# Kernel tuning notes

Measured on AMD Instinct MI355X. Metric: run time of the kernel, lower is better.

Reference implementation:

```python
import jax, jax.numpy as jnp
from jax import lax
import numpy as np

B, N, C_IN = 2, 4096, 64
NPOINT, K1, K2, S, K3 = 1024, 32, 16, 128, 16
C1, CD, CW1, CW2 = 64, 32, 96, 128


def _pw(x, W, b):
    # pointwise (1x1) conv + ReLU; x: (..., Cin), W: (Cout, Cin)
    return jax.nn.relu(jnp.einsum('...c,oc->...o', x, W) + b)


def _gather(x, idx):
    # x: (B, N, ...), idx: (B, ...) int -> fancy-gather along point dim
    return jax.vmap(lambda a, i: a[i])(x, idx)


def _fps(xyz, m):
    # furthest point sampling -> (B, m) int32 indices (non-differentiable)
    xyz = lax.stop_gradient(xyz)
    b, n, _ = xyz.shape
    d0 = jnp.full((b, n), 1e10, xyz.dtype)
    i0 = jnp.zeros((b,), jnp.int32)

    def body(carry, _):
        dists, last = carry
        lp = jnp.take_along_axis(xyz, last[:, None, None], axis=1)  # (B,1,3)
        dists = jnp.minimum(dists, jnp.sum((xyz - lp) ** 2, axis=-1))
        nxt = jnp.argmax(dists, axis=-1).astype(jnp.int32)
        return (dists, nxt), nxt

    (_, _), rest = lax.scan(body, (d0, i0), None, length=m - 1)
    return jnp.concatenate([i0[None, :], rest], axis=0).T  # (B,m)


def _knn(ref, q, k, ref_comp=None, q_comp=None):
    # k nearest ref points for each query point; optional same-component
    # constraint (knnquery with comp) via large distance penalty.
    ref = lax.stop_gradient(ref)
    q = lax.stop_gradient(q)
    d = jnp.sum((q[:, :, None, :] - ref[:, None, :, :]) ** 2, axis=-1)  # (B,M,N)
    if ref_comp is not None:
        d = d + jnp.where(q_comp[:, :, None] != ref_comp[:, None, :], 1e9, 0.0).astype(d.dtype)
    _, idx = lax.top_k(-d, k)
    return idx


def _indices(xyz, comp):
    cidx = _fps(xyz, NPOINT)                 # furthestsampling
    new_xyz = _gather(xyz, cidx)             # gathering
    new_comp = _gather(comp, cidx)
    idx1 = _knn(xyz, new_xyz, K1)            # grouper
    idx2 = _knn(new_xyz, new_xyz, K2, new_comp, new_comp)   # sp_knnquery
    sp_idx = _fps(new_xyz, S)
    sp_xyz = _gather(new_xyz, sp_idx)
    sp_comp = _gather(new_comp, sp_idx)
    idx_sp = _knn(new_xyz, sp_xyz, K3, new_comp, sp_comp)   # sp_knnquery_for_3rd
    idx3 = _knn(new_xyz, new_xyz, K2, new_comp, new_comp)   # sp_knnquery3
    return cidx, new_comp, idx1, idx2, idx_sp, idx3


def _forward(xyz, features, cidx, idx1, idx2, idx_sp, idx3, p):
    new_xyz = _gather(xyz, cidx)                             # (B,M,3)
    feat1 = _pw(features, p['W1d'], p['b1d'])                # mlps_1d -> (B,N,C1)
    center = _gather(feat1, cidx)                            # (B,M,C1)

    # --- stage 1: grouper over raw points ---
    d_xyz1 = _gather(xyz, idx1) - new_xyz[:, :, None, :]     # (B,M,K1,3)
    o_fea1 = _gather(feat1, idx1)                            # (B,M,K1,C1)
    w1 = _pw(jnp.concatenate([d_xyz1, o_fea1 - center[:, :, None, :]], -1), p['Ww1'], p['bw1'])
    c_fea1 = w1.max(axis=2)                                  # maxpool over K1
    w1s = jax.nn.softmax(w1, axis=2)                         # softmax over neighbors
    d1m = _pw(d_xyz1, p['Wdx1'], p['bdx1'])
    g_fea1 = jnp.sum(jnp.concatenate([d1m, o_fea1], -1) * w1s, axis=2)   # (B,M,96)

    # --- stage 2: comp-constrained knn among sampled points ---
    d_xyz2 = _gather(new_xyz, idx2) - new_xyz[:, :, None, :]  # (B,M,K2,3)
    o_fea2 = _gather(g_fea1, idx2)                            # (B,M,K2,96)
    d_fea2 = jnp.concatenate([o_fea2 - g_fea1[:, :, None, :], d_xyz2], -1)  # (B,M,K2,99)
    d2m = _pw(d_xyz2, p['Wdx2'], p['bdx2'])
    w2 = _pw(d_fea2, p['Ww2'], p['bw2'])                      # (B,M,K2,128)
    c_fea2 = w2.max(axis=2)
    w2s = jax.nn.softmax(w2, axis=2)
    g_fea2 = jnp.sum(jnp.concatenate([d2m, o_fea2], -1) * w2s, axis=2)   # (B,M,128)

    # --- stage 3: superpoint pooling, dense point<->superpoint attention ---
    sp_fea = _gather(c_fea2, idx_sp).max(axis=2)              # (B,S,128)
    d_fea3 = sp_fea[:, None, :, :] - c_fea2[:, :, None, :]    # (B,M,S,128)
    w3 = _pw(d_fea3, p['Ww3'], p['bw3'])
    w3s = jax.nn.softmax(w3, axis=2)                          # softmax over S
    g_fea3 = jnp.sum(c_fea2[:, :, None, :] * w3s, axis=2)     # (B,M,128)

    # --- stage 3b: knn group over g_fea2 ---
    d_xyz3 = _gather(new_xyz, idx3) - new_xyz[:, :, None, :]
    o_fea3 = _gather(g_fea2, idx3)
    d_fea3b = jnp.concatenate([o_fea3 - g_fea2[:, :, None, :], d_xyz3], -1)  # (B,M,K2,131)
    local_point_fea = _pw(d_fea3b, p['Wsp3'], p['bsp3']).max(axis=2)         # (B,M,128)

    fea3 = jnp.concatenate([g_fea3, local_point_fea, g_fea2, c_fea2, g_fea1, c_fea1, center], -1)  # (B,M,768)
    new_features = _pw(fea3, p['Wnew'], p['bnew'])            # (B,M,256)
    return new_xyz, jnp.swapaxes(new_features, 1, 2)          # (B,256,M) channel-first like torch


def setup_inputs():
    key = jax.random.key(0)
    ks = jax.random.split(key, 12)
    w = lambda k, s: jax.random.normal(k, s, jnp.float32) * 0.1
    return {
        'xyz': jax.random.normal(ks[0], (B, N, 3), jnp.float32),
        'features': jax.random.normal(ks[1], (B, N, C_IN), jnp.float32),
        'comp': jax.random.randint(ks[2], (B, N), 0, 8, jnp.int32),
        'W1d': w(ks[3], (C1, C_IN)), 'b1d': jnp.zeros((C1,), jnp.float32),
        'Wdx1': w(ks[4], (CD, 3)), 'bdx1': jnp.zeros((CD,), jnp.float32),
        'Ww1': w(ks[5], (CW1, 3 + C1)), 'bw1': jnp.zeros((CW1,), jnp.float32),
        'Wdx2': w(ks[6], (CD, 3)), 'bdx2': jnp.zeros((CD,), jnp.float32),
        'Ww2': w(ks[7], (CW2, CW1 + 3)), 'bw2': jnp.zeros((CW2,), jnp.float32),
        'Ww3': w(ks[8], (CW2, CW2)), 'bw3': jnp.zeros((CW2,), jnp.float32),
        'Wsp3': w(ks[9], (CW2, CW2 + 3)), 'bsp3': jnp.zeros((CW2,), jnp.float32),
        'Wnew': w(ks[10], (256, 4 * CW2 + 2 * CW1 + C1)), 'bnew': jnp.zeros((256,), jnp.float32),
    }


def reference(xyz, features, comp, W1d, b1d, Wdx1, bdx1, Ww1, bw1, Wdx2, bdx2, Ww2, bw2, Ww3, bw3, Wsp3, bsp3, Wnew, bnew):
    p = {'W1d': W1d, 'b1d': b1d, 'Wdx1': Wdx1, 'bdx1': bdx1, 'Ww1': Ww1, 'bw1': bw1,
         'Wdx2': Wdx2, 'bdx2': bdx2, 'Ww2': Ww2, 'bw2': bw2, 'Ww3': Ww3, 'bw3': bw3,
         'Wsp3': Wsp3, 'bsp3': bsp3, 'Wnew': Wnew, 'bnew': bnew}
    cidx, new_comp, idx1, idx2, idx_sp, idx3 = _indices(xyz, comp)
    new_xyz, new_features = _forward(xyz, features, cidx, idx1, idx2, idx_sp, idx3, p)
    return new_xyz, new_features, new_comp
```

## Files before the change

### kernel.cpp

```cpp
#include <hip/hip_runtime.h>
#include <hip/hip_bf16.h>

#define B_   2
#define N_   4096
#define M_   1024
#define K1_  32
#define K2_  16
#define C1_  64
#define CW1_ 96
#define CW2_ 128
#define CO_  256
#define F3_  768


__device__ __forceinline__ float dist3e(float ax, float ay, float az,
                                        float bx, float by, float bz) {
    float dx = __fsub_rn(ax, bx);
    float dy = __fsub_rn(ay, by);
    float dz = __fsub_rn(az, bz);
    return __fadd_rn(__fadd_rn(__fmul_rn(dx, dx), __fmul_rn(dy, dy)), __fmul_rn(dz, dz));
}

#define DPP_F32_MAX(v, ctrl)                                                        \
    (v) = fmaxf((v), __int_as_float(__builtin_amdgcn_update_dpp(                    \
              __float_as_int(v), __float_as_int(v), (ctrl), 0xf, 0xf, false)))
#define DPP_U32_MIN(v, ctrl)                                                        \
    {                                                                               \
        unsigned _t = (unsigned)__builtin_amdgcn_update_dpp(                        \
            (int)(v), (int)(v), (ctrl), 0xf, 0xf, false);                           \
        (v) = (v) < _t ? (v) : _t;                                                  \
    }

__device__ __forceinline__ float wave_max_f32(float v) {
    DPP_F32_MAX(v, 0x111);
    DPP_F32_MAX(v, 0x112);
    DPP_F32_MAX(v, 0x114);
    DPP_F32_MAX(v, 0x118);
    DPP_F32_MAX(v, 0x142);
    DPP_F32_MAX(v, 0x143);
    return __int_as_float(__builtin_amdgcn_readlane(__float_as_int(v), 63));
}

__device__ __forceinline__ unsigned wave_min_u32(unsigned v) {
    DPP_U32_MIN(v, 0x111);
    DPP_U32_MIN(v, 0x112);
    DPP_U32_MIN(v, 0x114);
    DPP_U32_MIN(v, 0x118);
    DPP_U32_MIN(v, 0x142);
    DPP_U32_MIN(v, 0x143);
    return (unsigned)__builtin_amdgcn_readlane((int)v, 63);
}

__global__ __launch_bounds__(512) void k_fps(const float* __restrict__ xyz,
        const int* __restrict__ comp, int* __restrict__ cidx,
        float* __restrict__ newxyz, int* __restrict__ newcomp,
        float* __restrict__ out_xyz, float* __restrict__ out_comp) {
    __shared__ float sx[N_], sy[N_], sz[N_];
    __shared__ unsigned long long spk[2][8];
    __shared__ int scid[M_];
    const int b = blockIdx.x;
    const int t = threadIdx.x;
    const int lane = t & 63, wv = t >> 6;
    const float* xb = xyz + (size_t)b * N_ * 3;
    for (int i = t; i < N_; i += 512) {
        sx[i] = xb[i * 3 + 0];
        sy[i] = xb[i * 3 + 1];
        sz[i] = xb[i * 3 + 2];
    }
    if (t == 0) scid[0] = 0;
    __syncthreads();
    float px[8], py[8], pz[8], pd[8];
    #pragma unroll
    for (int j = 0; j < 8; ++j) {
        const int p = j * 512 + t;
        px[j] = sx[p]; py[j] = sy[p]; pz[j] = sz[p];
        pd[j] = 1e10f;
    }
    int last = 0;
    for (int it = 1; it < M_; ++it) {
        const float lx = sx[last], ly = sy[last], lz = sz[last];
        #pragma unroll
        for (int j = 0; j < 8; ++j)
            pd[j] = fminf(pd[j], dist3e(px[j], py[j], pz[j], lx, ly, lz));
        float bd = pd[0]; int bj = 0;
        #pragma unroll
        for (int j = 1; j < 8; ++j) if (pd[j] > bd) { bd = pd[j]; bj = j; }
        const int bi = bj * 512 + t;
        const float mw = wave_max_f32(bd);
        unsigned cand = (bd == mw) ? (unsigned)bi : 0xffffffffu;
        const unsigned wi = wave_min_u32(cand);
        const int pb = it & 1;
        if (lane == 0)
            spk[pb][wv] = ((unsigned long long)__float_as_uint(mw) << 32) | (unsigned)(~wi);
        __syncthreads();
        unsigned long long g = spk[pb][0];
        #pragma unroll
        for (int w = 1; w < 8; ++w) {
            const unsigned long long x = spk[pb][w];
            g = x > g ? x : g;
        }
        last = (int)(~(unsigned)(g & 0xffffffffULL));
        if (t == 0) scid[it] = last;
    }
    __syncthreads();
    for (int m = t; m < M_; m += 512) {
        const int idx = scid[m];
        cidx[b * M_ + m] = idx;
        const float vx = sx[idx], vy = sy[idx], vz = sz[idx];
        newxyz[(size_t)(b * M_ + m) * 3 + 0] = vx;
        newxyz[(size_t)(b * M_ + m) * 3 + 1] = vy;
        newxyz[(size_t)(b * M_ + m) * 3 + 2] = vz;
        out_xyz[(size_t)(b * M_ + m) * 3 + 0] = vx;
        out_xyz[(size_t)(b * M_ + m) * 3 + 1] = vy;
        out_xyz[(size_t)(b * M_ + m) * 3 + 2] = vz;
        const int c = comp[b * N_ + idx];
        newcomp[b * M_ + m] = c;
        out_comp[b * M_ + m] = (float)c;
    }
}

__global__ __launch_bounds__(256) void k_feat1(const float* __restrict__ feats,
        const float* __restrict__ W1d, const float* __restrict__ b1d,
        float* __restrict__ feat1) {
    __shared__ float swt[C1_][C1_];
    __shared__ float sxr[4][C1_];
    const int t = threadIdx.x;
    const int o = t & 63, r = t >> 6;
    const size_t rb = (size_t)blockIdx.x * 4;
    for (int i = t; i < C1_ * C1_; i += 256) swt[i & 63][i >> 6] = W1d[i];
    for (int i = t; i < 4 * C1_; i += 256)
        sxr[i >> 6][i & 63] = feats[(rb + (i >> 6)) * C1_ + (i & 63)];
    __syncthreads();
    float acc = b1d[o];
    #pragma unroll
    for (int c = 0; c < C1_; ++c) acc += sxr[r][c] * swt[c][o];
    feat1[(rb + r) * C1_ + o] = fmaxf(acc, 0.f);
}

__global__ __launch_bounds__(256) void k_knn1(const float* __restrict__ xyz,
        const float* __restrict__ newxyz, int* __restrict__ idx1) {
    __shared__ float sx[N_], sy[N_], sz[N_];
    const int b = blockIdx.y;
    const int t = threadIdx.x, lane = t & 63, wv = t >> 6;
    const float* xb = xyz + (size_t)b * N_ * 3;
    for (int i = t; i < N_; i += 256) {
        sx[i] = xb[i * 3 + 0]; sy[i] = xb[i * 3 + 1]; sz[i] = xb[i * 3 + 2];
    }
    __syncthreads();
    const int m = blockIdx.x * 4 + wv;
    const float qx = newxyz[(size_t)(b * M_ + m) * 3 + 0];
    const float qy = newxyz[(size_t)(b * M_ + m) * 3 + 1];
    const float qz = newxyz[(size_t)(b * M_ + m) * 3 + 2];
    unsigned long long dp[64];
    #pragma unroll
    for (int j = 0; j < 64; ++j) {
        const int p = j * 64 + lane;
        const float v = dist3e(sx[p], sy[p], sz[p], qx, qy, qz);
        dp[j] = ((unsigned long long)__float_as_uint(v) << 32) | (unsigned)(p + 1);
    }
    unsigned long long lastk = 0ULL;
    int* op = idx1 + (size_t)(b * M_ + m) * K1_;
    for (int pass = 0; pass < K1_; ++pass) {
        unsigned long long best = ~0ULL;
        #pragma unroll
        for (int j = 0; j < 64; ++j) {
            const unsigned long long x = dp[j];
            if (x > lastk && x < best) best = x;
        }
        #pragma unroll
        for (int s = 32; s; s >>= 1) {
            const unsigned long long o2 = __shfl_xor(best, s, 64);
            best = o2 < best ? o2 : best;
        }
        if (lane == 0) op[pass] = (int)((unsigned)(best & 0xffffffffULL)) - 1;
        lastk = best;
    }
}

__global__ __launch_bounds__(256) void k_knn2(const float* __restrict__ newxyz,
        const int* __restrict__ newcomp, int* __restrict__ idx2) {
    __shared__ float sx[M_], sy[M_], sz[M_];
    __shared__ int scp[M_];
    const int b = blockIdx.y;
    const int t = threadIdx.x, lane = t & 63, wv = t >> 6;
    for (int i = t; i < M_; i += 256) {
        sx[i] = newxyz[(size_t)(b * M_ + i) * 3 + 0];
        sy[i] = newxyz[(size_t)(b * M_ + i) * 3 + 1];
        sz[i] = newxyz[(size_t)(b * M_ + i) * 3 + 2];
        scp[i] = newcomp[b * M_ + i];
    }
    __syncthreads();
    const int m = blockIdx.x * 4 + wv;
    const float qx = sx[m], qy = sy[m], qz = sz[m];
    const int qc = scp[m];
    unsigned long long dp[16];
    #pragma unroll
    for (int j = 0; j < 16; ++j) {
        const int p = j * 64 + lane;
        float dd = dist3e(sx[p], sy[p], sz[p], qx, qy, qz);
        if (scp[p] != qc) dd = __fadd_rn(dd, 1e9f);
        dp[j] = ((unsigned long long)__float_as_uint(dd) << 32) | (unsigned)(p + 1);
    }
    unsigned long long lastk = 0ULL;
    int* op = idx2 + (size_t)(b * M_ + m) * K2_;
    for (int pass = 0; pass < K2_; ++pass) {
        unsigned long long best = ~0ULL;
        #pragma unroll
        for (int j = 0; j < 16; ++j) {
            const unsigned long long x = dp[j];
            if (x > lastk && x < best) best = x;
        }
        #pragma unroll
        for (int s = 32; s; s >>= 1) {
            const unsigned long long o2 = __shfl_xor(best, s, 64);
            best = o2 < best ? o2 : best;
        }
        if (lane == 0) op[pass] = (int)((unsigned)(best & 0xffffffffULL)) - 1;
        lastk = best;
    }
}

__global__ __launch_bounds__(128) void k_stage1(const float* __restrict__ xyz,
        const float* __restrict__ feat1, const float* __restrict__ newxyz,
        const int* __restrict__ cidx, const int* __restrict__ idx1,
        const float* __restrict__ Ww1, const float* __restrict__ bw1,
        const float* __restrict__ Wdx1, const float* __restrict__ bdx1,
        float* __restrict__ gfea1, float* __restrict__ cfea1) {
    __shared__ float sdx[K1_][3];
    __shared__ float sof[K1_][C1_];
    __shared__ float sdf[K1_][C1_];
    __shared__ float sct[C1_];
    const int bm = blockIdx.x;
    const int b = bm >> 10;
    const int t = threadIdx.x;
    const int* iq = idx1 + (size_t)bm * K1_;
    const int ci = cidx[bm];
    if (t < C1_) sct[t] = feat1[((size_t)b * N_ + ci) * C1_ + t];
    for (int i = t; i < K1_ * C1_; i += 128) {
        const int k = i >> 6, c = i & 63;
        sof[k][c] = feat1[((size_t)b * N_ + iq[k]) * C1_ + c];
    }
    const float qx = newxyz[(size_t)bm * 3 + 0];
    const float qy = newxyz[(size_t)bm * 3 + 1];
    const float qz = newxyz[(size_t)bm * 3 + 2];
    if (t < K1_ * 3) {
        const int k = t / 3, c = t % 3;
        const float q = (c == 0) ? qx : ((c == 1) ? qy : qz);
        sdx[k][c] = xyz[((size_t)b * N_ + iq[k]) * 3 + c] - q;
    }
    __syncthreads();
    for (int i = t; i < K1_ * C1_; i += 128) {
        const int k = i >> 6, c = i & 63;
        sdf[k][c] = sof[k][c] - sct[c];
    }
    __syncthreads();
    const int o = t;
    if (o < CW1_) {
        float wr[67];
        const float* wp = Ww1 + o * 67;
        #pragma unroll
        for (int j = 0; j < 67; ++j) wr[j] = wp[j];
        const float bias = bw1[o];
        float w1v[K1_];
        #pragma unroll
        for (int k = 0; k < K1_; ++k) {
            float acc = bias + sdx[k][0] * wr[0] + sdx[k][1] * wr[1] + sdx[k][2] * wr[2];
            #pragma unroll
            for (int c = 0; c < C1_; ++c) acc += sdf[k][c] * wr[3 + c];
            w1v[k] = fmaxf(acc, 0.f);
        }
        float mx = w1v[0];
        #pragma unroll
        for (int k = 1; k < K1_; ++k) mx = fmaxf(mx, w1v[k]);
        cfea1[(size_t)bm * CW1_ + o] = mx;
        float dw0 = 0.f, dw1 = 0.f, dw2 = 0.f, db = 0.f;
        if (o < 32) {
            dw0 = Wdx1[o * 3 + 0]; dw1 = Wdx1[o * 3 + 1]; dw2 = Wdx1[o * 3 + 2];
            db = bdx1[o];
        }
        float s = 0.f, acc = 0.f;
        #pragma unroll
        for (int k = 0; k < K1_; ++k) {
            const float e = __expf(w1v[k] - mx);
            s += e;
            float val;
            if (o < 32) val = fmaxf(db + sdx[k][0] * dw0 + sdx[k][1] * dw1 + sdx[k][2] * dw2, 0.f);
            else        val = sof[k][o - 32];
            acc += val * e;
        }
        gfea1[(size_t)bm * CW1_ + o] = acc / s;
    }
}

__global__ __launch_bounds__(128) void k_stage2(const float* __restrict__ newxyz,
        const float* __restrict__ gfea1, const int* __restrict__ idx2,
        const float* __restrict__ Ww2, const float* __restrict__ bw2,
        const float* __restrict__ Wdx2, const float* __restrict__ bdx2,
        float* __restrict__ gfea2, float* __restrict__ cfea2) {
    __shared__ float sdx[K2_][3];
    __shared__ float sof[K2_][CW1_];
    __shared__ float sdf[K2_][CW1_];
    __shared__ float sg1[CW1_];
    const int bm = blockIdx.x;
    const int b = bm >> 10;
    const int t = threadIdx.x;
    const int* iq = idx2 + (size_t)bm * K2_;
    if (t < CW1_) sg1[t] = gfea1[(size_t)bm * CW1_ + t];
    for (int i = t; i < K2_ * CW1_; i += 128) {
        const int k = i / CW1_, c = i % CW1_;
        sof[k][c] = gfea1[((size_t)b * M_ + iq[k]) * CW1_ + c];
    }
    const float qx = newxyz[(size_t)bm * 3 + 0];
    const float qy = newxyz[(size_t)bm * 3 + 1];
    const float qz = newxyz[(size_t)bm * 3 + 2];
    if (t < K2_ * 3) {
        const int k = t / 3, c = t % 3;
        const float q = (c == 0) ? qx : ((c == 1) ? qy : qz);
        sdx[k][c] = newxyz[((size_t)b * M_ + iq[k]) * 3 + c] - q;
    }
    __syncthreads();
    for (int i = t; i < K2_ * CW1_; i += 128) {
        const int k = i / CW1_, c = i % CW1_;
        sdf[k][c] = sof[k][c] - sg1[c];
    }
    __syncthreads();
    const int o = t;
    float wr[99];
    const float* wp = Ww2 + o * 99;
    #pragma unroll
    for (int j = 0; j < 99; ++j) wr[j] = wp[j];
    const float bias = bw2[o];
    float wv[K2_];
    #pragma unroll
    for (int k = 0; k < K2_; ++k) {
        float acc = bias;
        #pragma unroll
        for (int c = 0; c < CW1_; ++c) acc += sdf[k][c] * wr[c];
        acc += sdx[k][0] * wr[96] + sdx[k][1] * wr[97] + sdx[k][2] * wr[98];
        wv[k] = fmaxf(acc, 0.f);
    }
    float mx = wv[0];
    #pragma unroll
    for (int k = 1; k < K2_; ++k) mx = fmaxf(mx, wv[k]);
    cfea2[(size_t)bm * CW2_ + o] = mx;
    float dw0 = 0.f, dw1 = 0.f, dw2 = 0.f, db = 0.f;
    if (o < 32) {
        dw0 = Wdx2[o * 3 + 0]; dw1 = Wdx2[o * 3 + 1]; dw2 = Wdx2[o * 3 + 2];
        db = bdx2[o];
    }
    float s = 0.f, acc = 0.f;
    #pragma unroll
    for (int k = 0; k < K2_; ++k) {
        const float e = __expf(wv[k] - mx);
        s += e;
        float val;
        if (o < 32) val = fmaxf(db + sdx[k][0] * dw0 + sdx[k][1] * dw1 + sdx[k][2] * dw2, 0.f);
        else        val = sof[k][o - 32];
        acc += val * e;
    }
    gfea2[(size_t)bm * CW2_ + o] = acc / s;
}

__global__ __launch_bounds__(128) void k_stage3b(const float* __restrict__ newxyz,
        const float* __restrict__ gfea2, const int* __restrict__ idx2,
        const float* __restrict__ Wsp3, const float* __restrict__ bsp3,
        float* __restrict__ locf) {
    __shared__ float sdx[K2_][3];
    __shared__ float sdf[K2_][CW2_];
    __shared__ float sg2[CW2_];
    const int bm = blockIdx.x;
    const int b = bm >> 10;
    const int t = threadIdx.x;
    const int* iq = idx2 + (size_t)bm * K2_;
    sg2[t] = gfea2[(size_t)bm * CW2_ + t];
    const float qx = newxyz[(size_t)bm * 3 + 0];
    const float qy = newxyz[(size_t)bm * 3 + 1];
    const float qz = newxyz[(size_t)bm * 3 + 2];
    if (t < K2_ * 3) {
        const int k = t / 3, c = t % 3;
        const float q = (c == 0) ? qx : ((c == 1) ? qy : qz);
        sdx[k][c] = newxyz[((size_t)b * M_ + iq[k]) * 3 + c] - q;
    }
    __syncthreads();
    for (int i = t; i < K2_ * CW2_; i += 128) {
        const int k = i >> 7, c = i & 127;
        sdf[k][c] = gfea2[((size_t)b * M_ + iq[k]) * CW2_ + c] - sg2[c];
    }
    __syncthreads();
    const int o = t;
    float wr[131];
    const float* wp = Wsp3 + o * 131;
    #pragma unroll
    for (int j = 0; j < 131; ++j) wr[j] = wp[j];
    const float bias = bsp3[o];
    float mx = 0.f;
    #pragma unroll
    for (int k = 0; k < K2_; ++k) {
        float acc = bias;
        #pragma unroll
        for (int c = 0; c < CW2_; ++c) acc += sdf[k][c] * wr[c];
        acc += sdx[k][0] * wr[128] + sdx[k][1] * wr[129] + sdx[k][2] * wr[130];
        mx = fmaxf(mx, acc);
    }
    locf[(size_t)bm * CW2_ + o] = mx;
}

__global__ __launch_bounds__(256) void k_final(const float* __restrict__ cfea2,
        const float* __restrict__ locf, const float* __restrict__ gfea2,
        const float* __restrict__ gfea1, const float* __restrict__ cfea1,
        const float* __restrict__ feat1, const int* __restrict__ cidx,
        const float* __restrict__ Wnew, const float* __restrict__ bnew,
        float* __restrict__ out_feat) {
    __shared__ float sf[8][F3_];
    const int t = threadIdx.x;
    const int qb = blockIdx.x * 8;
    for (int i = t; i < 8 * F3_; i += 256) {
        const int q = i / F3_, j = i % F3_;
        const int bm = qb + q;
        float v;
        if (j < 128)      v = cfea2[(size_t)bm * CW2_ + j];
        else if (j < 256) v = locf [(size_t)bm * CW2_ + (j - 128)];
        else if (j < 384) v = gfea2[(size_t)bm * CW2_ + (j - 256)];
        else if (j < 512) v = cfea2[(size_t)bm * CW2_ + (j - 384)];
        else if (j < 608) v = gfea1[(size_t)bm * CW1_ + (j - 512)];
        else if (j < 704) v = cfea1[(size_t)bm * CW1_ + (j - 608)];
        else { const int b = bm >> 10; v = feat1[((size_t)b * N_ + cidx[bm]) * C1_ + (j - 704)]; }
        sf[q][j] = v;
    }
    __syncthreads();
    const int o = t;
    const float bias = bnew[o];
    float acc[8];
    #pragma unroll
    for (int q = 0; q < 8; ++q) acc[q] = bias;
    const float* wp = Wnew + (size_t)o * F3_;
    for (int j = 0; j < F3_; ++j) {
        const float w = wp[j];
        #pragma unroll
        for (int q = 0; q < 8; ++q) acc[q] += sf[q][j] * w;
    }
    #pragma unroll
    for (int q = 0; q < 8; ++q) {
        const int bm = qb + q;
        const int b = bm >> 10, m = bm & (M_ - 1);
        out_feat[((size_t)b * CO_ + o) * M_ + m] = fmaxf(acc[q], 0.f);
    }
}

extern "C" void kernel_launch(void* const* d_in, const int* in_sizes, int n_in,
                              void* d_out, int out_size, void* d_ws, size_t ws_size,
                              hipStream_t stream) {
    const float* xyz   = (const float*)d_in[0];
    const float* feats = (const float*)d_in[1];
    const int*   comp  = (const int*)d_in[2];
    const float* W1d  = (const float*)d_in[3];
    const float* b1d  = (const float*)d_in[4];
    const float* Wdx1 = (const float*)d_in[5];
    const float* bdx1 = (const float*)d_in[6];
    const float* Ww1  = (const float*)d_in[7];
    const float* bw1  = (const float*)d_in[8];
    const float* Wdx2 = (const float*)d_in[9];
    const float* bdx2 = (const float*)d_in[10];
    const float* Ww2  = (const float*)d_in[11];
    const float* bw2  = (const float*)d_in[12];
    const float* Wsp3 = (const float*)d_in[15];
    const float* bsp3 = (const float*)d_in[16];
    const float* Wnew = (const float*)d_in[17];
    const float* bnew = (const float*)d_in[18];

    float* out      = (float*)d_out;
    float* out_xyz  = out;
    float* out_feat = out + (size_t)B_ * M_ * 3;
    float* out_comp = out + (size_t)B_ * M_ * 3 + (size_t)B_ * CO_ * M_;

    char* wsp = (char*)d_ws;
    auto alloc = [&](size_t bytes) {
        char* p = wsp;
        wsp += (bytes + 255) & ~(size_t)255;
        return (void*)p;
    };
    int*   cidx    = (int*)  alloc((size_t)B_ * M_ * 4);
    float* newxyz  = (float*)alloc((size_t)B_ * M_ * 3 * 4);
    int*   newcomp = (int*)  alloc((size_t)B_ * M_ * 4);
    float* feat1   = (float*)alloc((size_t)B_ * N_ * C1_ * 4);
    int*   idx1    = (int*)  alloc((size_t)B_ * M_ * K1_ * 4);
    int*   idx2    = (int*)  alloc((size_t)B_ * M_ * K2_ * 4);
    float* gfea1   = (float*)alloc((size_t)B_ * M_ * CW1_ * 4);
    float* cfea1   = (float*)alloc((size_t)B_ * M_ * CW1_ * 4);
    float* gfea2   = (float*)alloc((size_t)B_ * M_ * CW2_ * 4);
    float* cfea2   = (float*)alloc((size_t)B_ * M_ * CW2_ * 4);
    float* locf    = (float*)alloc((size_t)B_ * M_ * CW2_ * 4);

    k_fps<<<dim3(B_), dim3(512), 0, stream>>>(xyz, comp, cidx, newxyz, newcomp,
                                              out_xyz, out_comp);
    k_feat1<<<dim3(B_ * N_ / 4), dim3(256), 0, stream>>>(feats, W1d, b1d, feat1);
    k_knn1<<<dim3(M_ / 4, B_), dim3(256), 0, stream>>>(xyz, newxyz, idx1);
    k_knn2<<<dim3(M_ / 4, B_), dim3(256), 0, stream>>>(newxyz, newcomp, idx2);
    k_stage1<<<dim3(B_ * M_), dim3(128), 0, stream>>>(xyz, feat1, newxyz, cidx, idx1,
                                                      Ww1, bw1, Wdx1, bdx1, gfea1, cfea1);
    k_stage2<<<dim3(B_ * M_), dim3(128), 0, stream>>>(newxyz, gfea1, idx2,
                                                      Ww2, bw2, Wdx2, bdx2, gfea2, cfea2);
    k_stage3b<<<dim3(B_ * M_), dim3(128), 0, stream>>>(newxyz, gfea2, idx2, Wsp3, bsp3, locf);
    k_final<<<dim3(B_ * M_ / 8), dim3(256), 0, stream>>>(cfea2, locf, gfea2, gfea1, cfea1,
                                                         feat1, cidx, Wnew, bnew, out_feat);
}
```

Measured before the change: 987.5 us.

## Fuse feat1 into FPS launch, carry winner coords, use DPP wave-min in KNN

Merges the feat1 pointwise conv into the FPS kernel as extra blocks, so the conv runs concurrently with the two long serial FPS blocks instead of after them. Inside FPS, the winning lane publishes its point's coordinates along with the key, which removes the dependent shared-memory lookup of the last point at the start of each iteration. The KNN kernels replace the 64-bit shuffle butterfly with two 32-bit DPP wave-min reductions (distance, then index). The price is a larger shared-memory union and 512-thread feat1 blocks, plus slightly more work per FPS iteration for the coordinate select.

Result: slower. 1.219 ms (+23.5%).

```diff
diff --git a/kernel.cpp b/kernel.cpp
--- a/kernel.cpp
+++ b/kernel.cpp
@@ -32,42 +32,63 @@
     }
 
 __device__ __forceinline__ float wave_max_f32(float v) {
-    DPP_F32_MAX(v, 0x111);
-    DPP_F32_MAX(v, 0x112);
-    DPP_F32_MAX(v, 0x114);
-    DPP_F32_MAX(v, 0x118);
-    DPP_F32_MAX(v, 0x142);
-    DPP_F32_MAX(v, 0x143);
+    DPP_F32_MAX(v, 0x111); DPP_F32_MAX(v, 0x112); DPP_F32_MAX(v, 0x114);
+    DPP_F32_MAX(v, 0x118); DPP_F32_MAX(v, 0x142); DPP_F32_MAX(v, 0x143);
     return __int_as_float(__builtin_amdgcn_readlane(__float_as_int(v), 63));
 }
 
 __device__ __forceinline__ unsigned wave_min_u32(unsigned v) {
-    DPP_U32_MIN(v, 0x111);
-    DPP_U32_MIN(v, 0x112);
-    DPP_U32_MIN(v, 0x114);
-    DPP_U32_MIN(v, 0x118);
-    DPP_U32_MIN(v, 0x142);
-    DPP_U32_MIN(v, 0x143);
+    DPP_U32_MIN(v, 0x111); DPP_U32_MIN(v, 0x112); DPP_U32_MIN(v, 0x114);
+    DPP_U32_MIN(v, 0x118); DPP_U32_MIN(v, 0x142); DPP_U32_MIN(v, 0x143);
     return (unsigned)__builtin_amdgcn_readlane((int)v, 63);
 }
 
-__global__ __launch_bounds__(512) void k_fps(const float* __restrict__ xyz,
+union SMemFused {
+    struct {
+        float sx[N_], sy[N_], sz[N_];
+        unsigned long long sk[2][8];
+        float4 sc[2][8];
+        int scid[M_];
+    } fps;
+    struct {
+        float swt[C1_][C1_];
+        float sxr[8][C1_];
+    } f1;
+};
+
+__global__ __launch_bounds__(512) void k_fps_feat1(const float* __restrict__ xyz,
         const int* __restrict__ comp, int* __restrict__ cidx,
         float* __restrict__ newxyz, int* __restrict__ newcomp,
-        float* __restrict__ out_xyz, float* __restrict__ out_comp) {
-    __shared__ float sx[N_], sy[N_], sz[N_];
-    __shared__ unsigned long long spk[2][8];
-    __shared__ int scid[M_];
+        float* __restrict__ out_xyz, float* __restrict__ out_comp,
+        const float* __restrict__ feats, const float* __restrict__ W1d,
+        const float* __restrict__ b1d, float* __restrict__ feat1) {
+    __shared__ SMemFused sm;
+    const int t = threadIdx.x;
+
+    if (blockIdx.x >= B_) {
+        const int o = t & 63, r = t >> 6;
+        const size_t rb = (size_t)(blockIdx.x - B_) * 8;
+        for (int i = t; i < C1_ * C1_; i += 512) sm.f1.swt[i & 63][i >> 6] = W1d[i];
+        for (int i = t; i < 8 * C1_; i += 512)
+            sm.f1.sxr[i >> 6][i & 63] = feats[(rb + (i >> 6)) * C1_ + (i & 63)];
+        __syncthreads();
+        float acc = b1d[o];
+        #pragma unroll
+        for (int c = 0; c < C1_; ++c) acc += sm.f1.sxr[r][c] * sm.f1.swt[c][o];
+        feat1[(rb + r) * C1_ + o] = fmaxf(acc, 0.f);
+        return;
+    }
+
     const int b = blockIdx.x;
-    const int t = threadIdx.x;
     const int lane = t & 63, wv = t >> 6;
+    float* sx = sm.fps.sx; float* sy = sm.fps.sy; float* sz = sm.fps.sz;
     const float* xb = xyz + (size_t)b * N_ * 3;
     for (int i = t; i < N_; i += 512) {
         sx[i] = xb[i * 3 + 0];
         sy[i] = xb[i * 3 + 1];
         sz[i] = xb[i * 3 + 2];
     }
-    if (t == 0) scid[0] = 0;
+    if (t == 0) sm.fps.scid[0] = 0;
     __syncthreads();
     float px[8], py[8], pz[8], pd[8];
     #pragma unroll
@@ -76,9 +97,8 @@
         px[j] = sx[p]; py[j] = sy[p]; pz[j] = sz[p];
         pd[j] = 1e10f;
     }
-    int last = 0;
+    float lx = sx[0], ly = sy[0], lz = sz[0];
     for (int it = 1; it < M_; ++it) {
-        const float lx = sx[last], ly = sy[last], lz = sz[last];
         #pragma unroll
         for (int j = 0; j < 8; ++j)
             pd[j] = fminf(pd[j], dist3e(px[j], py[j], pz[j], lx, ly, lz));
@@ -86,25 +106,34 @@
         #pragma unroll
         for (int j = 1; j < 8; ++j) if (pd[j] > bd) { bd = pd[j]; bj = j; }
         const int bi = bj * 512 + t;
+        float bx = px[0], by = py[0], bz = pz[0];
+        #pragma unroll
+        for (int j = 1; j < 8; ++j)
+            if (bj == j) { bx = px[j]; by = py[j]; bz = pz[j]; }
         const float mw = wave_max_f32(bd);
         unsigned cand = (bd == mw) ? (unsigned)bi : 0xffffffffu;
         const unsigned wi = wave_min_u32(cand);
         const int pb = it & 1;
-        if (lane == 0)
-            spk[pb][wv] = ((unsigned long long)__float_as_uint(mw) << 32) | (unsigned)(~wi);
+        if ((unsigned)bi == wi) {
+            sm.fps.sk[pb][wv] =
+                ((unsigned long long)__float_as_uint(bd) << 32) | (unsigned)(~bi);
+            sm.fps.sc[pb][wv] = make_float4(bx, by, bz, 0.f);
+        }
         __syncthreads();
-        unsigned long long g = spk[pb][0];
+        unsigned long long g = sm.fps.sk[pb][0];
+        float4 gc = sm.fps.sc[pb][0];
         #pragma unroll
         for (int w = 1; w < 8; ++w) {
-            const unsigned long long x = spk[pb][w];
-            g = x > g ? x : g;
-        }
-        last = (int)(~(unsigned)(g & 0xffffffffULL));
-        if (t == 0) scid[it] = last;
+            const unsigned long long x = sm.fps.sk[pb][w];
+            const float4 xc = sm.fps.sc[pb][w];
+            if (x > g) { g = x; gc = xc; }
+        }
+        lx = gc.x; ly = gc.y; lz = gc.z;
+        if (t == 0) sm.fps.scid[it] = (int)(~(unsigned)(g & 0xffffffffULL));
     }
     __syncthreads();
     for (int m = t; m < M_; m += 512) {
-        const int idx = scid[m];
+        const int idx = sm.fps.scid[m];
         cidx[b * M_ + m] = idx;
         const float vx = sx[idx], vy = sy[idx], vz = sz[idx];
         newxyz[(size_t)(b * M_ + m) * 3 + 0] = vx;
@@ -119,24 +148,6 @@
     }
 }
 
-__global__ __launch_bounds__(256) void k_feat1(const float* __restrict__ feats,
-        const float* __restrict__ W1d, const float* __restrict__ b1d,
-        float* __restrict__ feat1) {
-    __shared__ float swt[C1_][C1_];
-    __shared__ float sxr[4][C1_];
-    const int t = threadIdx.x;
-    const int o = t & 63, r = t >> 6;
-    const size_t rb = (size_t)blockIdx.x * 4;
-    for (int i = t; i < C1_ * C1_; i += 256) swt[i & 63][i >> 6] = W1d[i];
-    for (int i = t; i < 4 * C1_; i += 256)
-        sxr[i >> 6][i & 63] = feats[(rb + (i >> 6)) * C1_ + (i & 63)];
-    __syncthreads();
-    float acc = b1d[o];
-    #pragma unroll
-    for (int c = 0; c < C1_; ++c) acc += sxr[r][c] * swt[c][o];
-    feat1[(rb + r) * C1_ + o] = fmaxf(acc, 0.f);
-}
-
 __global__ __launch_bounds__(256) void k_knn1(const float* __restrict__ xyz,
         const float* __restrict__ newxyz, int* __restrict__ idx1) {
     __shared__ float sx[N_], sy[N_], sz[N_];
@@ -167,12 +178,12 @@
             const unsigned long long x = dp[j];
             if (x > lastk && x < best) best = x;
         }
-        #pragma unroll
-        for (int s = 32; s; s >>= 1) {
-            const unsigned long long o2 = __shfl_xor(best, s, 64);
-            best = o2 < best ? o2 : best;
-        }
-        if (lane == 0) op[pass] = (int)((unsigned)(best & 0xffffffffULL)) - 1;
+        const unsigned hi = (unsigned)(best >> 32);
+        const unsigned minhi = wave_min_u32(hi);
+        unsigned lo = (hi == minhi) ? (unsigned)best : 0xffffffffu;
+        const unsigned minlo = wave_min_u32(lo);
+        best = ((unsigned long long)minhi << 32) | minlo;
+        if (lane == 0) op[pass] = (int)minlo - 1;
         lastk = best;
     }
 }
@@ -210,12 +221,12 @@
             const unsigned long long x = dp[j];
             if (x > lastk && x < best) best = x;
         }
-        #pragma unroll
-        for (int s = 32; s; s >>= 1) {
-            const unsigned long long o2 = __shfl_xor(best, s, 64);
-            best = o2 < best ? o2 : best;
-        }
-        if (lane == 0) op[pass] = (int)((unsigned)(best & 0xffffffffULL)) - 1;
+        const unsigned hi = (unsigned)(best >> 32);
+        const unsigned minhi = wave_min_u32(hi);
+        unsigned lo = (hi == minhi) ? (unsigned)best : 0xffffffffu;
+        const unsigned minlo = wave_min_u32(lo);
+        best = ((unsigned long long)minhi << 32) | minlo;
+        if (lane == 0) op[pass] = (int)minlo - 1;
         lastk = best;
     }
 }
@@ -491,9 +502,9 @@
     float* cfea2   = (float*)alloc((size_t)B_ * M_ * CW2_ * 4);
     float* locf    = (float*)alloc((size_t)B_ * M_ * CW2_ * 4);
 
-    k_fps<<<dim3(B_), dim3(512), 0, stream>>>(xyz, comp, cidx, newxyz, newcomp,
-                                              out_xyz, out_comp);
-    k_feat1<<<dim3(B_ * N_ / 4), dim3(256), 0, stream>>>(feats, W1d, b1d, feat1);
+    k_fps_feat1<<<dim3(B_ + B_ * N_ / 8), dim3(512), 0, stream>>>(
+        xyz, comp, cidx, newxyz, newcomp, out_xyz, out_comp,
+        feats, W1d, b1d, feat1);
     k_knn1<<<dim3(M_ / 4, B_), dim3(256), 0, stream>>>(xyz, newxyz, idx1);
     k_knn2<<<dim3(M_ / 4, B_), dim3(256), 0, stream>>>(newxyz, newcomp, idx2);
     k_stage1<<<dim3(B_ * M_), dim3(128), 0, stream>>>(xyz, feat1, newxyz, cidx, idx1,
```
